# Kernel tuning notes

Hardware: AMD Instinct MI355X
Metric: run time of the kernel (lower is better)

Reference implementation:

```python
import jax, jax.numpy as jnp
import numpy as np

# Constants from init_kwargs
DT = 0.01
NIV = 8          # energy_input_dim[1]
HID = 64         # hidden_dims[0]
FEAT = 501       # per-field microstructure feature length (501+501=1002)


def _lin(k, fin, fout):
    return jax.random.normal(k, (fin, fout), dtype=jnp.float32) / np.sqrt(fin)


def setup_inputs() -> dict:
    key = jax.random.key(0)
    ks = jax.random.split(key, 12)
    B, T = 8192, 512
    e = jax.random.normal(ks[0], (B, T, 1), dtype=jnp.float32) * 0.1
    e_dot = jax.random.normal(ks[1], (B, T, 1), dtype=jnp.float32) * 0.1
    # positive microstructure fields (code computes nu**-1 and E/nu**2)
    E = jax.random.uniform(ks[2], (B, FEAT), minval=0.5, maxval=2.0, dtype=jnp.float32)
    nu = jax.random.uniform(ks[3], (B, FEAT), minval=0.5, maxval=2.0, dtype=jnp.float32)
    return {
        "e": e, "e_dot": e_dot, "E": E, "nu": nu,
        # EnergyFunction.B : Linear(1002,64) -> ReLU -> Linear(64,niv)
        "Bw1": _lin(ks[4], 2 * FEAT, HID), "Bb1": jnp.zeros((HID,), jnp.float32),
        "Bw2": _lin(ks[5], HID, NIV), "Bb2": jnp.zeros((NIV,), jnp.float32),
        # InverseDissipationPotential.beta : Linear(1002,64)->Softplus->Linear(64,niv)->Softplus
        "bw1": _lin(ks[6], 2 * FEAT, HID), "bb1": jnp.zeros((HID,), jnp.float32),
        "bw2": _lin(ks[7], HID, NIV), "bb2": jnp.zeros((NIV,), jnp.float32),
    }


def reference(e, e_dot, E, nu, Bw1, Bb1, Bw2, Bb2, bw1, bb1, bw2, bb2):
    # --- microstructure encoder (TrueFeatures) ---
    nu_p = 1.0 / jnp.mean(1.0 / nu, axis=1, keepdims=True)                 # [B,1]
    E_p = jnp.mean(E / nu ** 2, axis=1, keepdims=True) * nu_p ** 2         # [B,1]
    m = jnp.concatenate([E, nu], axis=-1)                                  # [B,1002]

    # Time-invariant MLP coefficients (hoisted out of the time loop)
    Bm = jax.nn.relu(m @ Bw1 + Bb1) @ Bw2 + Bb2                            # [B,NIV]
    beta = jax.nn.softplus(jax.nn.softplus(m @ bw1 + bb1) @ bw2 + bb2)     # [B,NIV]
    Bsum = jnp.sum(Bm, axis=-1, keepdims=True)                             # [B,1]

    B_, niv = Bm.shape
    xi0 = jnp.zeros((B_, niv), dtype=e.dtype)

    def step(xi, inp):
        u, p = inp                                                          # [B,1],[B,1]
        # Analytic gradients of L = sum_{b,k} Bm_bk * (0.5*E' u^2 + 0.5*(u-xi_k)^2 + 0.5*sum_j xi_j^2)
        du = u - xi                                                         # [B,NIV]
        grad_u = Bsum * E_p * u + jnp.sum(Bm * du, axis=-1, keepdims=True)  # [B,1] (s_eq)
        grad_v = -Bm * du + Bsum * xi                                       # [B,NIV] (d)
        q = -grad_v
        # Analytic gradients of potential = -0.5*nu' p^2 + 0.5*sum(beta*q^2)
        grad_p = -nu_p * p                                                  # [B,1] (s_neq)
        grad_q = beta * q                                                   # [B,NIV] (kinetics)
        stress = grad_u - grad_p
        return xi + DT * grad_q, (stress, xi)

    xs = (jnp.swapaxes(e, 0, 1), jnp.swapaxes(e_dot, 0, 1))                 # [T,B,1]
    _, (stress_t, xi_t) = jax.lax.scan(step, xi0, xs)
    stress = jnp.swapaxes(stress_t, 0, 1)                                   # [B,T,1]
    xi = jnp.swapaxes(xi_t, 0, 1)                                           # [B,T,NIV]
    return stress, xi
```

## Files before the change

### kernel.cpp

```cpp
#include <hip/hip_runtime.h>
#include <hip/hip_bf16.h>

#define FEATN 501
#define KPAD 1024
#define MSTRIDE 1032
#define NB 8192
#define NT 512
#define DTC 0.01f

typedef __attribute__((ext_vector_type(8))) short short8;
typedef __attribute__((ext_vector_type(4))) short short4v;
typedef __attribute__((ext_vector_type(4))) float f32x4;

__device__ __forceinline__ float softplus_f(float x) {
    return fmaxf(x, 0.f) + log1pf(expf(-fabsf(x)));
}
__device__ __forceinline__ ushort f2bf(float x) {
    __hip_bfloat16 h = __float2bfloat16(x);
    return *reinterpret_cast<ushort*>(&h);
}
__device__ __forceinline__ void gl_lds16(const void* g, void* l) {
    __builtin_amdgcn_global_load_lds(
        (const __attribute__((address_space(1))) void*)g,
        (__attribute__((address_space(3))) void*)l, 16, 0, 0);
}
__device__ __forceinline__ float dpp_add(float x, const int ctrl) {
    int s = __builtin_bit_cast(int, x);
    int y;
    switch (ctrl) {
    case 0xB1:  y = __builtin_amdgcn_update_dpp(0, s, 0xB1, 0xf, 0xf, true); break;
    case 0x4E:  y = __builtin_amdgcn_update_dpp(0, s, 0x4E, 0xf, 0xf, true); break;
    default:    y = __builtin_amdgcn_update_dpp(0, s, 0x141, 0xf, 0xf, true); break;
    }
    return x + __builtin_bit_cast(float, y);
}

__global__ __launch_bounds__(256) void wtrans_kernel(
    const float* __restrict__ Bw1, const float* __restrict__ bw1,
    ushort* __restrict__ Wt) {
    const int h = blockIdx.x;
    const int lane = threadIdx.x & 63;
    const int wv = threadIdx.x >> 6;
    const float* W = (h < 64) ? Bw1 : bw1;
    const int col = h & 63;
    #pragma unroll
    for (int it = 0; it < 4; ++it) {
        const int k = it * 256 + wv * 64 + lane;
        const int ksrc = (k < FEATN) ? k
                       : (k >= 512 && k < 512 + FEATN) ? k - 11 : -1;
        const float v = (ksrc >= 0) ? W[(size_t)ksrc * 64 + col] : 0.f;
        Wt[(size_t)h * KPAD + k] = f2bf(v);
    }
}

__global__ __launch_bounds__(1024, 8) void enc_kernel(
    const float* __restrict__ E, const float* __restrict__ nu,
    const ushort* __restrict__ Wt,
    const float* __restrict__ Bb1, const float* __restrict__ bb1,
    const float* __restrict__ Bw2, const float* __restrict__ Bb2,
    const float* __restrict__ bw2, const float* __restrict__ bb2,
    float* __restrict__ xi) {
    __shared__ ushort Ml[16 * MSTRIDE];
    __shared__ float red[3][2048];
    __shared__ float hid[128][17];
    __shared__ float nups[16], Eps[16];

    const int tid = threadIdx.x;
    const int w = tid >> 6, lane = tid & 63;
    const int bb0 = blockIdx.x * 16;

    {
        const int bl = w;
        const size_t base = (size_t)(bb0 + bl) * FEATN;
        float s1 = 0.f, s2 = 0.f;
        #pragma unroll
        for (int it = 0; it < 2; ++it) {
            const int i0 = it * 256 + lane * 4;
            if (i0 + 3 < FEATN) {
                const float4 Ev = *(const float4*)(E + base + i0);
                const float4 nv = *(const float4*)(nu + base + i0);
                const float i0v = 1.0f / nv.x, i1v = 1.0f / nv.y;
                const float i2v = 1.0f / nv.z, i3v = 1.0f / nv.w;
                s1 += (i0v + i1v) + (i2v + i3v);
                s2 = fmaf(Ev.x, i0v * i0v, s2);
                s2 = fmaf(Ev.y, i1v * i1v, s2);
                s2 = fmaf(Ev.z, i2v * i2v, s2);
                s2 = fmaf(Ev.w, i3v * i3v, s2);
                short4v ep = {(short)f2bf(Ev.x), (short)f2bf(Ev.y),
                              (short)f2bf(Ev.z), (short)f2bf(Ev.w)};
                short4v np_ = {(short)f2bf(nv.x), (short)f2bf(nv.y),
                               (short)f2bf(nv.z), (short)f2bf(nv.w)};
                *(short4v*)&Ml[bl * MSTRIDE + i0] = ep;
                *(short4v*)&Ml[bl * MSTRIDE + 512 + i0] = np_;
            } else if (i0 < FEATN) {
                const float Ev = E[base + i0];
                const float nv = nu[base + i0];
                const float iv = 1.0f / nv;
                s1 += iv;
                s2 = fmaf(Ev, iv * iv, s2);
                Ml[bl * MSTRIDE + i0] = f2bf(Ev);
                Ml[bl * MSTRIDE + 512 + i0] = f2bf(nv);
            }
        }
        if (lane < 11) {
            Ml[bl * MSTRIDE + FEATN + lane] = 0;
            Ml[bl * MSTRIDE + 512 + FEATN + lane] = 0;
        }
        #pragma unroll
        for (int o = 32; o; o >>= 1) {
            s1 += __shfl_xor(s1, o);
            s2 += __shfl_xor(s2, o);
        }
        if (lane == 0) {
            const float np = (float)FEATN / s1;
            nups[bl] = np;
            Eps[bl] = (s2 / (float)FEATN) * np * np;
        }
    }
    __syncthreads();

    const int g = w & 3, q = w >> 2;
    const int r15 = lane & 15, kg = lane >> 4;
    const ushort* wp0 = Wt + (size_t)(g * 32 + r15) * KPAD + q * 256 + kg * 8;
    const ushort* wp1 = wp0 + 16 * KPAD;
    const int boff = r15 * MSTRIDE + q * 256 + kg * 8;

    f32x4 acc0 = {0.f, 0.f, 0.f, 0.f}, acc1 = acc0;
    #pragma unroll
    for (int s = 0; s < 8; ++s) {
        const int kb = s * 32;
        const short8 a0 = *(const short8*)(wp0 + kb);
        const short8 a1 = *(const short8*)(wp1 + kb);
        const short8 b = *(const short8*)&Ml[boff + kb];
        acc0 = __builtin_amdgcn_mfma_f32_16x16x32_bf16(a0, b, acc0, 0, 0, 0);
        acc1 = __builtin_amdgcn_mfma_f32_16x16x32_bf16(a1, b, acc1, 0, 0, 0);
    }

    if (q > 0) {
        *(f32x4*)&red[q - 1][(g * 64 + lane) * 8] = acc0;
        *(f32x4*)&red[q - 1][(g * 64 + lane) * 8 + 4] = acc1;
    }
    __syncthreads();
    if (q == 0) {
        #pragma unroll
        for (int p = 0; p < 3; ++p) {
            acc0 += *(const f32x4*)&red[p][(g * 64 + lane) * 8];
            acc1 += *(const f32x4*)&red[p][(g * 64 + lane) * 8 + 4];
        }
        #pragma unroll
        for (int t = 0; t < 2; ++t) {
            #pragma unroll
            for (int r = 0; r < 4; ++r) {
                const int h = g * 32 + t * 16 + kg * 4 + r;
                const float bias = (h < 64) ? Bb1[h] : bb1[h - 64];
                float v = (t ? acc1[r] : acc0[r]) + bias;
                v = (h < 64) ? fmaxf(v, 0.f) : softplus_f(v);
                hid[h][r15] = v;
            }
        }
    }
    __syncthreads();

    if (tid < 128) {
        const int bl = tid >> 3, k = tid & 7;
        float dB = 0.f, db = 0.f;
        #pragma unroll 8
        for (int h = 0; h < 64; ++h) {
            dB = fmaf(hid[h][bl], Bw2[h * 8 + k], dB);
            db = fmaf(hid[64 + h][bl], bw2[h * 8 + k], db);
        }
        const float Bm = dB + Bb2[k];
        const float be = softplus_f(db + bb2[k]);
        float Bs = Bm;
        Bs += __shfl_xor(Bs, 1);
        Bs += __shfl_xor(Bs, 2);
        Bs += __shfl_xor(Bs, 4);
        float* cb = xi + (size_t)(bb0 + bl) * 4096;
        cb[k] = 1.f - DTC * be * (Bm + Bs);
        cb[8 + k] = DTC * be * Bm;
        cb[16 + k] = Bm;
        if (k == 0) { cb[24] = Bs * Eps[bl]; cb[25] = nups[bl]; }
    }
}

__global__ __launch_bounds__(256) void time_kernel(
    const float* __restrict__ e, const float* __restrict__ ed,
    const float* coef, float* stress, float* xi_out) {
    __shared__ float els[4][512];
    __shared__ float pls[4][512];
    __shared__ float scr[4][256];
    const int wv = threadIdx.x >> 6;
    const int wid = (blockIdx.x << 2) + wv;
    const int lane = threadIdx.x & 63;
    const int j = lane >> 3, k = lane & 7;

    const float* eb = e + (size_t)wid * NT;
    const float* edb = ed + (size_t)wid * NT;
    gl_lds16(eb + lane * 4, &els[wv][0]);
    gl_lds16(eb + 256 + lane * 4, &els[wv][256]);
    gl_lds16(edb + lane * 4, &pls[wv][0]);
    gl_lds16(edb + 256 + lane * 4, &pls[wv][256]);

    const float* cb = coef + (size_t)wid * 4096;
    const float a = cb[k];
    const float c = cb[8 + k];
    const float Bm = cb[16 + k];
    const float sE = cb[24];
    const float nup = cb[25];
    asm volatile("s_waitcnt vmcnt(0)" ::: "memory");

    const float a2 = a * a, a4 = a2 * a2;
    float A = 1.f;
    if (j & 1) A *= a;
    if (j & 2) A *= a2;
    if (j & 4) A *= a4;
    float pw[8];
    {
        float run = c;
        #pragma unroll
        for (int i = 7; i >= 0; --i) {
            const bool on = (i < j);
            pw[i] = on ? run : 0.f;
            run = on ? run * a : run;
        }
    }

    float* xb = xi_out + (size_t)wid * (NT * 8);
    float* sb = stress + (size_t)wid * NT;
    const float* el = &els[wv][0];
    const float* pl = &pls[wv][0];

    float4 q0 = *(const float4*)(el);
    float4 q1 = *(const float4*)(el + 4);
    float uj = el[j];
    float pj = pl[j];

    float xs = 0.f;
    for (int g = 0; g < 16; ++g) {
        const int T0 = g * 32;
        float vx[4], sv[4];
        #pragma unroll
        for (int w = 0; w < 4; ++w) {
            const int t0 = T0 + w * 8;
            const float u0 = q0.x, u1 = q0.y, u2 = q0.z, u3 = q0.w;
            const float u4 = q1.x, u5 = q1.y, u6 = q1.z, u7 = q1.w;
            const float cuj = uj, cpj = pj;
            if (t0 + 8 < NT) {
                q0 = *(const float4*)(el + t0 + 8);
                q1 = *(const float4*)(el + t0 + 12);
                uj = el[t0 + 8 + j];
                pj = pl[t0 + 8 + j];
            }
            float xi_j = A * xs;
            xi_j = fmaf(pw[0], u0, xi_j);
            xi_j = fmaf(pw[1], u1, xi_j);
            xi_j = fmaf(pw[2], u2, xi_j);
            xi_j = fmaf(pw[3], u3, xi_j);
            xi_j = fmaf(pw[4], u4, xi_j);
            xi_j = fmaf(pw[5], u5, xi_j);
            xi_j = fmaf(pw[6], u6, xi_j);
            xi_j = fmaf(pw[7], u7, xi_j);
            vx[w] = xi_j;
            float r = Bm * (cuj - xi_j);
            r = dpp_add(r, 0xB1);
            r = dpp_add(r, 0x4E);
            r = dpp_add(r, 0x141);
            sv[w] = fmaf(sE, cuj, fmaf(nup, cpj, r));
            xs = fmaf(a, __shfl(xi_j, 56 + k), c * u7);
        }
        #pragma unroll
        for (int w = 0; w < 4; ++w) scr[wv][w * 64 + lane] = vx[w];
        *(float4*)(xb + T0 * 8 + lane * 4) =
            *(const float4*)&scr[wv][lane * 4];
        if (k == 0) {
            #pragma unroll
            for (int w = 0; w < 4; ++w) scr[wv][w * 8 + j] = sv[w];
        }
        if (lane < 8)
            *(float4*)(sb + T0 + lane * 4) =
                *(const float4*)&scr[wv][lane * 4];
    }
}

extern "C" void kernel_launch(void* const* d_in, const int* in_sizes, int n_in,
                              void* d_out, int out_size, void* d_ws, size_t ws_size,
                              hipStream_t stream) {
    const float* e   = (const float*)d_in[0];
    const float* ed  = (const float*)d_in[1];
    const float* E   = (const float*)d_in[2];
    const float* nu  = (const float*)d_in[3];
    const float* Bw1 = (const float*)d_in[4];
    const float* Bb1 = (const float*)d_in[5];
    const float* Bw2 = (const float*)d_in[6];
    const float* Bb2 = (const float*)d_in[7];
    const float* bw1 = (const float*)d_in[8];
    const float* bb1 = (const float*)d_in[9];
    const float* bw2 = (const float*)d_in[10];
    const float* bb2 = (const float*)d_in[11];

    float* out = (float*)d_out;
    float* stress = out;
    float* xi = out + (size_t)NB * NT;
    ushort* Wt = (ushort*)out;

    wtrans_kernel<<<128, 256, 0, stream>>>(Bw1, bw1, Wt);
    enc_kernel<<<512, 1024, 0, stream>>>(E, nu, Wt, Bb1, bb1,
                                         Bw2, Bb2, bw2, bb2, xi);
    time_kernel<<<2048, 256, 0, stream>>>(e, ed, xi, stress, xi);
}
```

Before: 67.23 us.

## Retile weight layout, move coefficients to workspace, simplify time-loop stores

Several changes land together. The transposed weight matrix is stored in a k-block-major tiled layout in the workspace so MFMA A-operand loads are contiguous. Per-batch coefficients move from the xi output buffer into a compact 32-float workspace slot. The encoder's vectorized feature load is replaced by a simple strided scalar loop. The time loop is fully unrolled and writes xi and stress directly with per-lane stores instead of staging through LDS. The stress formula is algebraically refolded (Bs*(Eps+1), minus Bm·xi) to save a subtract per step. The per-lane scalar stores may coalesce worse than the previous float4 writes.

```diff
diff --git a/kernel.cpp b/kernel.cpp
--- a/kernel.cpp
+++ b/kernel.cpp
@@ -9,7 +9,6 @@
 #define DTC 0.01f
 
 typedef __attribute__((ext_vector_type(8))) short short8;
-typedef __attribute__((ext_vector_type(4))) short short4v;
 typedef __attribute__((ext_vector_type(4))) float f32x4;
 
 __device__ __forceinline__ float softplus_f(float x) {
@@ -39,17 +38,16 @@
     const float* __restrict__ Bw1, const float* __restrict__ bw1,
     ushort* __restrict__ Wt) {
     const int h = blockIdx.x;
-    const int lane = threadIdx.x & 63;
-    const int wv = threadIdx.x >> 6;
     const float* W = (h < 64) ? Bw1 : bw1;
     const int col = h & 63;
     #pragma unroll
     for (int it = 0; it < 4; ++it) {
-        const int k = it * 256 + wv * 64 + lane;
+        const int k = it * 256 + threadIdx.x;
         const int ksrc = (k < FEATN) ? k
                        : (k >= 512 && k < 512 + FEATN) ? k - 11 : -1;
         const float v = (ksrc >= 0) ? W[(size_t)ksrc * 64 + col] : 0.f;
-        Wt[(size_t)h * KPAD + k] = f2bf(v);
+        Wt[(size_t)(((k >> 5) * 128 + h) * 4 + ((k >> 3) & 3)) * 8 + (k & 7)] =
+            f2bf(v);
     }
 }
 
@@ -59,7 +57,7 @@
     const float* __restrict__ Bb1, const float* __restrict__ bb1,
     const float* __restrict__ Bw2, const float* __restrict__ Bb2,
     const float* __restrict__ bw2, const float* __restrict__ bb2,
-    float* __restrict__ xi) {
+    float* __restrict__ cw) {
     __shared__ ushort Ml[16 * MSTRIDE];
     __shared__ float red[3][2048];
     __shared__ float hid[128][17];
@@ -70,41 +68,20 @@
     const int bb0 = blockIdx.x * 16;
 
     {
-        const int bl = w;
-        const size_t base = (size_t)(bb0 + bl) * FEATN;
+        const size_t base = (size_t)(bb0 + w) * FEATN;
         float s1 = 0.f, s2 = 0.f;
-        #pragma unroll
-        for (int it = 0; it < 2; ++it) {
-            const int i0 = it * 256 + lane * 4;
-            if (i0 + 3 < FEATN) {
-                const float4 Ev = *(const float4*)(E + base + i0);
-                const float4 nv = *(const float4*)(nu + base + i0);
-                const float i0v = 1.0f / nv.x, i1v = 1.0f / nv.y;
-                const float i2v = 1.0f / nv.z, i3v = 1.0f / nv.w;
-                s1 += (i0v + i1v) + (i2v + i3v);
-                s2 = fmaf(Ev.x, i0v * i0v, s2);
-                s2 = fmaf(Ev.y, i1v * i1v, s2);
-                s2 = fmaf(Ev.z, i2v * i2v, s2);
-                s2 = fmaf(Ev.w, i3v * i3v, s2);
-                short4v ep = {(short)f2bf(Ev.x), (short)f2bf(Ev.y),
-                              (short)f2bf(Ev.z), (short)f2bf(Ev.w)};
-                short4v np_ = {(short)f2bf(nv.x), (short)f2bf(nv.y),
-                               (short)f2bf(nv.z), (short)f2bf(nv.w)};
-                *(short4v*)&Ml[bl * MSTRIDE + i0] = ep;
-                *(short4v*)&Ml[bl * MSTRIDE + 512 + i0] = np_;
-            } else if (i0 < FEATN) {
-                const float Ev = E[base + i0];
-                const float nv = nu[base + i0];
-                const float iv = 1.0f / nv;
-                s1 += iv;
-                s2 = fmaf(Ev, iv * iv, s2);
-                Ml[bl * MSTRIDE + i0] = f2bf(Ev);
-                Ml[bl * MSTRIDE + 512 + i0] = f2bf(nv);
-            }
+        for (int i = lane; i < FEATN; i += 64) {
+            const float Ev = E[base + i];
+            const float nv = nu[base + i];
+            const float inv = 1.0f / nv;
+            s1 += inv;
+            s2 = fmaf(Ev, inv * inv, s2);
+            Ml[w * MSTRIDE + i] = f2bf(Ev);
+            Ml[w * MSTRIDE + 512 + i] = f2bf(nv);
         }
         if (lane < 11) {
-            Ml[bl * MSTRIDE + FEATN + lane] = 0;
-            Ml[bl * MSTRIDE + 512 + FEATN + lane] = 0;
+            Ml[w * MSTRIDE + FEATN + lane] = 0;
+            Ml[w * MSTRIDE + 512 + FEATN + lane] = 0;
         }
         #pragma unroll
         for (int o = 32; o; o >>= 1) {
@@ -113,49 +90,49 @@
         }
         if (lane == 0) {
             const float np = (float)FEATN / s1;
-            nups[bl] = np;
-            Eps[bl] = (s2 / (float)FEATN) * np * np;
+            nups[w] = np;
+            Eps[w] = (s2 / (float)FEATN) * np * np;
         }
     }
     __syncthreads();
 
     const int g = w & 3, q = w >> 2;
     const int r15 = lane & 15, kg = lane >> 4;
-    const ushort* wp0 = Wt + (size_t)(g * 32 + r15) * KPAD + q * 256 + kg * 8;
-    const ushort* wp1 = wp0 + 16 * KPAD;
-    const int boff = r15 * MSTRIDE + q * 256 + kg * 8;
-
-    f32x4 acc0 = {0.f, 0.f, 0.f, 0.f}, acc1 = acc0;
-    #pragma unroll
-    for (int s = 0; s < 8; ++s) {
-        const int kb = s * 32;
-        const short8 a0 = *(const short8*)(wp0 + kb);
-        const short8 a1 = *(const short8*)(wp1 + kb);
-        const short8 b = *(const short8*)&Ml[boff + kb];
-        acc0 = __builtin_amdgcn_mfma_f32_16x16x32_bf16(a0, b, acc0, 0, 0, 0);
-        acc1 = __builtin_amdgcn_mfma_f32_16x16x32_bf16(a1, b, acc1, 0, 0, 0);
-    }
-
-    if (q > 0) {
-        *(f32x4*)&red[q - 1][(g * 64 + lane) * 8] = acc0;
-        *(f32x4*)&red[q - 1][(g * 64 + lane) * 8 + 4] = acc1;
-    }
-    __syncthreads();
-    if (q == 0) {
+    {
+        const ushort* wbase = Wt + (size_t)(q * 8) * 4096;
+        const int aoff = (g * 32 + r15) * 32 + kg * 8;
+        const int boff = r15 * MSTRIDE + q * 256 + kg * 8;
+
+        f32x4 acc0 = {0.f, 0.f, 0.f, 0.f}, acc1 = acc0;
         #pragma unroll
-        for (int p = 0; p < 3; ++p) {
-            acc0 += *(const f32x4*)&red[p][(g * 64 + lane) * 8];
-            acc1 += *(const f32x4*)&red[p][(g * 64 + lane) * 8 + 4];
-        }
-        #pragma unroll
-        for (int t = 0; t < 2; ++t) {
+        for (int s = 0; s < 8; ++s) {
+            const short8 a0 = *(const short8*)(wbase + s * 4096 + aoff);
+            const short8 a1 = *(const short8*)(wbase + s * 4096 + aoff + 512);
+            const short8 b = *(const short8*)&Ml[boff + s * 32];
+            acc0 = __builtin_amdgcn_mfma_f32_16x16x32_bf16(a0, b, acc0, 0, 0, 0);
+            acc1 = __builtin_amdgcn_mfma_f32_16x16x32_bf16(a1, b, acc1, 0, 0, 0);
+        }
+        if (q > 0) {
+            *(f32x4*)&red[q - 1][(g * 64 + lane) * 8] = acc0;
+            *(f32x4*)&red[q - 1][(g * 64 + lane) * 8 + 4] = acc1;
+        }
+        __syncthreads();
+        if (q == 0) {
             #pragma unroll
-            for (int r = 0; r < 4; ++r) {
-                const int h = g * 32 + t * 16 + kg * 4 + r;
-                const float bias = (h < 64) ? Bb1[h] : bb1[h - 64];
-                float v = (t ? acc1[r] : acc0[r]) + bias;
-                v = (h < 64) ? fmaxf(v, 0.f) : softplus_f(v);
-                hid[h][r15] = v;
+            for (int p = 0; p < 3; ++p) {
+                acc0 += *(const f32x4*)&red[p][(g * 64 + lane) * 8];
+                acc1 += *(const f32x4*)&red[p][(g * 64 + lane) * 8 + 4];
+            }
+            #pragma unroll
+            for (int t = 0; t < 2; ++t) {
+                #pragma unroll
+                for (int r = 0; r < 4; ++r) {
+                    const int h = g * 32 + t * 16 + kg * 4 + r;
+                    const float bias = (h < 64) ? Bb1[h] : bb1[h - 64];
+                    float v = (t ? acc1[r] : acc0[r]) + bias;
+                    v = (h < 64) ? fmaxf(v, 0.f) : softplus_f(v);
+                    hid[h][r15] = v;
+                }
             }
         }
     }
@@ -175,20 +152,23 @@
         Bs += __shfl_xor(Bs, 1);
         Bs += __shfl_xor(Bs, 2);
         Bs += __shfl_xor(Bs, 4);
-        float* cb = xi + (size_t)(bb0 + bl) * 4096;
+        float* cb = cw + (size_t)(bb0 + bl) * 32;
         cb[k] = 1.f - DTC * be * (Bm + Bs);
         cb[8 + k] = DTC * be * Bm;
         cb[16 + k] = Bm;
-        if (k == 0) { cb[24] = Bs * Eps[bl]; cb[25] = nups[bl]; }
+        if (k == 0) {
+            cb[24] = Bs * (Eps[bl] + 1.f);
+            cb[25] = nups[bl];
+        }
     }
 }
 
 __global__ __launch_bounds__(256) void time_kernel(
     const float* __restrict__ e, const float* __restrict__ ed,
-    const float* coef, float* stress, float* xi_out) {
+    const float* __restrict__ cw, float* __restrict__ stress,
+    float* __restrict__ xi_out) {
     __shared__ float els[4][512];
     __shared__ float pls[4][512];
-    __shared__ float scr[4][256];
     const int wv = threadIdx.x >> 6;
     const int wid = (blockIdx.x << 2) + wv;
     const int lane = threadIdx.x & 63;
@@ -201,11 +181,11 @@
     gl_lds16(edb + lane * 4, &pls[wv][0]);
     gl_lds16(edb + 256 + lane * 4, &pls[wv][256]);
 
-    const float* cb = coef + (size_t)wid * 4096;
+    const float* cb = cw + (size_t)wid * 32;
     const float a = cb[k];
     const float c = cb[8 + k];
     const float Bm = cb[16 + k];
-    const float sE = cb[24];
+    const float sE2 = cb[24];
     const float nup = cb[25];
     asm volatile("s_waitcnt vmcnt(0)" ::: "memory");
 
@@ -230,55 +210,31 @@
     const float* el = &els[wv][0];
     const float* pl = &pls[wv][0];
 
-    float4 q0 = *(const float4*)(el);
-    float4 q1 = *(const float4*)(el + 4);
-    float uj = el[j];
-    float pj = pl[j];
-
     float xs = 0.f;
-    for (int g = 0; g < 16; ++g) {
-        const int T0 = g * 32;
-        float vx[4], sv[4];
-        #pragma unroll
-        for (int w = 0; w < 4; ++w) {
-            const int t0 = T0 + w * 8;
-            const float u0 = q0.x, u1 = q0.y, u2 = q0.z, u3 = q0.w;
-            const float u4 = q1.x, u5 = q1.y, u6 = q1.z, u7 = q1.w;
-            const float cuj = uj, cpj = pj;
-            if (t0 + 8 < NT) {
-                q0 = *(const float4*)(el + t0 + 8);
-                q1 = *(const float4*)(el + t0 + 12);
-                uj = el[t0 + 8 + j];
-                pj = pl[t0 + 8 + j];
-            }
-            float xi_j = A * xs;
-            xi_j = fmaf(pw[0], u0, xi_j);
-            xi_j = fmaf(pw[1], u1, xi_j);
-            xi_j = fmaf(pw[2], u2, xi_j);
-            xi_j = fmaf(pw[3], u3, xi_j);
-            xi_j = fmaf(pw[4], u4, xi_j);
-            xi_j = fmaf(pw[5], u5, xi_j);
-            xi_j = fmaf(pw[6], u6, xi_j);
-            xi_j = fmaf(pw[7], u7, xi_j);
-            vx[w] = xi_j;
-            float r = Bm * (cuj - xi_j);
-            r = dpp_add(r, 0xB1);
-            r = dpp_add(r, 0x4E);
-            r = dpp_add(r, 0x141);
-            sv[w] = fmaf(sE, cuj, fmaf(nup, cpj, r));
-            xs = fmaf(a, __shfl(xi_j, 56 + k), c * u7);
-        }
-        #pragma unroll
-        for (int w = 0; w < 4; ++w) scr[wv][w * 64 + lane] = vx[w];
-        *(float4*)(xb + T0 * 8 + lane * 4) =
-            *(const float4*)&scr[wv][lane * 4];
-        if (k == 0) {
-            #pragma unroll
-            for (int w = 0; w < 4; ++w) scr[wv][w * 8 + j] = sv[w];
-        }
-        if (lane < 8)
-            *(float4*)(sb + T0 + lane * 4) =
-                *(const float4*)&scr[wv][lane * 4];
+    #pragma unroll
+    for (int it = 0; it < 64; ++it) {
+        const int t0 = it * 8;
+        const float4 q0 = *(const float4*)(el + t0);
+        const float4 q1 = *(const float4*)(el + t0 + 4);
+        const float cuj = el[t0 + j];
+        const float cpj = pl[t0 + j];
+        float xi_j = A * xs;
+        xi_j = fmaf(pw[0], q0.x, xi_j);
+        xi_j = fmaf(pw[1], q0.y, xi_j);
+        xi_j = fmaf(pw[2], q0.z, xi_j);
+        xi_j = fmaf(pw[3], q0.w, xi_j);
+        xi_j = fmaf(pw[4], q1.x, xi_j);
+        xi_j = fmaf(pw[5], q1.y, xi_j);
+        xi_j = fmaf(pw[6], q1.z, xi_j);
+        xi_j = fmaf(pw[7], q1.w, xi_j);
+        xb[t0 * 8 + lane] = xi_j;
+        float r = Bm * xi_j;
+        r = dpp_add(r, 0xB1);
+        r = dpp_add(r, 0x4E);
+        r = dpp_add(r, 0x141);
+        if (k == 0)
+            sb[t0 + j] = fmaf(cuj, sE2, fmaf(nup, cpj, -r));
+        xs = fmaf(a, __shfl(xi_j, 56 + k), c * q1.w);
     }
 }
 
@@ -301,10 +257,11 @@
     float* out = (float*)d_out;
     float* stress = out;
     float* xi = out + (size_t)NB * NT;
-    ushort* Wt = (ushort*)out;
+    ushort* Wt = (ushort*)d_ws;
+    float* cw = (float*)((char*)d_ws + (1 << 20));
 
     wtrans_kernel<<<128, 256, 0, stream>>>(Bw1, bw1, Wt);
     enc_kernel<<<512, 1024, 0, stream>>>(E, nu, Wt, Bb1, bb1,
-                                         Bw2, Bb2, bw2, bb2, xi);
-    time_kernel<<<2048, 256, 0, stream>>>(e, ed, xi, stress, xi);
-}
+                                         Bw2, Bb2, bw2, bb2, cw);
+    time_kernel<<<2048, 256, 0, stream>>>(e, ed, cw, stress, xi);
+}
```

Measured after the change: 60.64 us. 9.8% less time.
